# Performance work log

Hardware: AMD Instinct MI355X
Metric: run time of the kernel (lower is better)

Reference implementation:

```python
import jax, jax.numpy as jnp
import numpy as np

B, T, S, H = 8, 256, 256, 512

def setup_inputs() -> dict:
    key = jax.random.key(0)
    k1, k2, k3, k4, k5, k6 = jax.random.split(key, 6)
    query = jax.random.normal(k1, (B, T, H), dtype=jnp.float32)
    encoder_outputs = jax.random.normal(k2, (B, S, H), dtype=jnp.float32)
    # lengths in [1, S] so every row has at least one valid source position
    src_lengths = jax.random.randint(k3, (B,), 1, S + 1, dtype=jnp.int64)
    scale = 1.0 / np.sqrt(H)
    W_h = jax.random.normal(k4, (H, H), dtype=jnp.float32) * scale  # nn.Linear weight (out, in)
    W_s = jax.random.normal(k5, (H, H), dtype=jnp.float32) * scale
    v = jax.random.normal(k6, (H,), dtype=jnp.float32) * scale     # nn.Linear(H,1) weight squeezed
    return {"query": query, "encoder_outputs": encoder_outputs,
            "src_lengths": src_lengths, "W_h": W_h, "W_s": W_s, "v": v}

def reference(query, encoder_outputs, src_lengths, W_h, W_s, v):
    # Linear without bias: y = x @ W^T
    enc_f = jnp.einsum('bsh,oh->bso', encoder_outputs, W_h)   # (B,S,H)
    qry_f = jnp.einsum('bth,oh->bto', query, W_s)             # (B,T,H)
    # additive score: v^T tanh(enc_f + qry_f), broadcast over (T,S)
    scores = jnp.einsum('btsh,h->bts',
                        jnp.tanh(enc_f[:, None, :, :] + qry_f[:, :, None, :]), v)  # (B,T,S)
    mask = jnp.arange(S)[None, :] >= src_lengths[:, None]      # (B,S) True = pad
    scores = jnp.where(mask[:, None, :], -jnp.inf, scores)
    attn_weights = jax.nn.softmax(scores, axis=-1)             # (B,T,S)
    attn_out = jnp.einsum('bts,bsh->bth', attn_weights, encoder_outputs)
    return attn_out
```

## Files before the change

### kernel.cpp

```cpp
#include <hip/hip_runtime.h>
#include <cstddef>
#include <math.h>

#define BD 8
#define TD 256
#define SD 256
#define HD 512
#define K2F 2.885390081777927f

#define EXP2(x) __builtin_amdgcn_exp2f(x)
#define RCP(x)  __builtin_amdgcn_rcpf(x)

typedef __attribute__((ext_vector_type(8))) _Float16 half8;
typedef __attribute__((ext_vector_type(4))) float float4v;

__device__ __forceinline__ float exp2_sat(float x) {
    return EXP2(fminf(fmaxf(x, -80.0f), 80.0f));
}

#define LSTR 40
__global__ __launch_bounds__(256) void proj_kernel(
    const float* __restrict__ enc, const float* __restrict__ qry,
    const float* __restrict__ Wh,  const float* __restrict__ Ws,
    float* __restrict__ encT, float* __restrict__ qryf)
{
    __shared__ _Float16 LA[64 * LSTR], LB[64 * LSTR];

    const int tid = threadIdx.x;
    const int l = tid & 63, w = tid >> 6;
    const int rf = l & 15, q = l >> 4;
    const int my = blockIdx.y;
    const bool isq = my >= 32;
    const int m0 = my * 64;
    const int n0 = blockIdx.x * 64;

    const int srow = tid >> 2;
    const int scol = (tid & 3) * 8;
    const float* Abase = isq
        ? qry + (size_t)(m0 - 2048 + srow) * HD + scol
        : enc + (size_t)(m0 + srow) * HD + scol;
    const float* Bbase = (isq ? Ws : Wh) + (size_t)(n0 + srow) * HD + scol;

    const int mi = (w & 1) * 32, ni = (w >> 1) * 32;

    float4v acc[2][2] = {{{0,0,0,0},{0,0,0,0}},{{0,0,0,0},{0,0,0,0}}};

    float4 a0 = *(const float4*)(Abase);
    float4 a1 = *(const float4*)(Abase + 4);
    float4 b0 = *(const float4*)(Bbase);
    float4 b1 = *(const float4*)(Bbase + 4);

    for (int ks = 0; ks < 16; ++ks) {
        if (ks) __syncthreads();
        {
            float af[8] = {a0.x,a0.y,a0.z,a0.w,a1.x,a1.y,a1.z,a1.w};
            float bf[8] = {b0.x,b0.y,b0.z,b0.w,b1.x,b1.y,b1.z,b1.w};
            half8 ha, hb;
            #pragma unroll
            for (int i = 0; i < 8; ++i) { ha[i] = (_Float16)af[i]; hb[i] = (_Float16)bf[i]; }
            *(half8*)&LA[srow * LSTR + scol] = ha;
            *(half8*)&LB[srow * LSTR + scol] = hb;
        }
        __syncthreads();
        if (ks + 1 < 16) {
            const int ko = (ks + 1) * 32;
            a0 = *(const float4*)(Abase + ko);
            a1 = *(const float4*)(Abase + ko + 4);
            b0 = *(const float4*)(Bbase + ko);
            b1 = *(const float4*)(Bbase + ko + 4);
        }
        half8 ah[2], bh[2];
        #pragma unroll
        for (int i = 0; i < 2; ++i) {
            ah[i] = *(const half8*)&LA[(mi + i * 16 + rf) * LSTR + q * 8];
            bh[i] = *(const half8*)&LB[(ni + i * 16 + rf) * LSTR + q * 8];
        }
        #pragma unroll
        for (int i = 0; i < 2; ++i)
            #pragma unroll
            for (int j = 0; j < 2; ++j)
                acc[i][j] = __builtin_amdgcn_mfma_f32_16x16x32_f16(ah[i], bh[j], acc[i][j], 0, 0, 0);
    }

    if (!isq) {
        const int b  = m0 >> 8;
        const int sb = (m0 & 255) + mi + q * 4;
        float* base = encT + (size_t)b * HD * SD;
        #pragma unroll
        for (int i = 0; i < 2; ++i)
            #pragma unroll
            for (int j = 0; j < 2; ++j) {
                float4 o = make_float4(exp2_sat(acc[i][j][0]*K2F), exp2_sat(acc[i][j][1]*K2F),
                                       exp2_sat(acc[i][j][2]*K2F), exp2_sat(acc[i][j][3]*K2F));
                *(float4*)(base + (size_t)(n0 + ni + j * 16 + rf) * SD + sb + i * 16) = o;
            }
    } else {
        const int mrow = (m0 - 2048) + mi + q * 4;
        #pragma unroll
        for (int i = 0; i < 2; ++i)
            #pragma unroll
            for (int j = 0; j < 2; ++j)
                #pragma unroll
                for (int r = 0; r < 4; ++r)
                    qryf[(size_t)(mrow + i * 16 + r) * HD + n0 + ni + j * 16 + rf] =
                        exp2_sat(acc[i][j][r] * K2F);
    }
}

__global__ __launch_bounds__(512) void attn_kernel(
    const float* __restrict__ enc,
    const float* __restrict__ encT,
    const float* __restrict__ qry_f,
    const float* __restrict__ v,
    const int*   __restrict__ lens,
    float* __restrict__ out)
{
    __shared__ float qls[HD * 4];
    __shared__ float pls[8 * 4 * 256];
    __shared__ float wls[4 * SD];

    const int blk = blockIdx.x;
    const int b   = blk >> 6;
    const int t0  = (blk & 63) * 4;
    const int tid = threadIdx.x;
    const int w   = tid >> 6;
    const int l   = tid & 63;

    {
        const float* qf = qry_f + ((size_t)b * TD + t0) * HD;
        float4 qv;
        qv.x = qf[0 * HD + tid]; qv.y = qf[1 * HD + tid];
        qv.z = qf[2 * HD + tid]; qv.w = qf[3 * HD + tid];
        *(float4*)&qls[tid * 4] = qv;
    }
    __syncthreads();

    float a[4][4];
    #pragma unroll
    for (int t = 0; t < 4; ++t)
        #pragma unroll
        for (int c = 0; c < 4; ++c) a[t][c] = 0.0f;
    {
        const float* ep = encT + (size_t)b * HD * SD + (size_t)(w * 64) * SD + l * 4;
        const int jbase = w * 64;
        float4 e = *(const float4*)ep;
        #pragma unroll 2
        for (int jj = 0; jj < 64; ++jj) {
            float4 en = *(const float4*)(ep + (size_t)(jj + 1) * SD);
            float4 q4 = *(const float4*)&qls[(jbase + jj) * 4];
            float vj = v[jbase + jj];
            float ev[4] = {e.x, e.y, e.z, e.w};
            float qv[4] = {q4.x, q4.y, q4.z, q4.w};
            #pragma unroll
            for (int t = 0; t < 4; ++t)
                #pragma unroll
                for (int c = 0; c < 4; ++c) {
                    float p = fmaf(ev[c], qv[t], 1.0f);
                    a[t][c] = fmaf(vj, RCP(p), a[t][c]);
                }
            e = en;
        }
    }
    #pragma unroll
    for (int t = 0; t < 4; ++t)
        *(float4*)&pls[(w * 4 + t) * 256 + l * 4] = make_float4(a[t][0], a[t][1], a[t][2], a[t][3]);
    __syncthreads();

    if (w < 4) {
        const int t = w;
        float p[4] = {0, 0, 0, 0};
        #pragma unroll
        for (int g = 0; g < 8; ++g) {
            float4 pp = *(const float4*)&pls[(g * 4 + t) * 256 + l * 4];
            p[0] += pp.x; p[1] += pp.y; p[2] += pp.z; p[3] += pp.w;
        }
        const int len = lens[b];
        const int s0 = l * 4;
        float sc[4];
        #pragma unroll
        for (int c = 0; c < 4; ++c)
            sc[c] = (s0 + c < len) ? -2.0f * p[c] : -INFINITY;
        float mx = fmaxf(fmaxf(sc[0], sc[1]), fmaxf(sc[2], sc[3]));
        #pragma unroll
        for (int off = 32; off; off >>= 1) mx = fmaxf(mx, __shfl_xor(mx, off));
        float ex[4]; float sum = 0.0f;
        #pragma unroll
        for (int c = 0; c < 4; ++c) { ex[c] = __expf(sc[c] - mx); sum += ex[c]; }
        #pragma unroll
        for (int off = 32; off; off >>= 1) sum += __shfl_xor(sum, off);
        const float inv = RCP(sum);
        *(float4*)&wls[t * SD + s0] = make_float4(ex[0]*inv, ex[1]*inv, ex[2]*inv, ex[3]*inv);
    }
    __syncthreads();

    const int g  = tid >> 7;
    const int h4 = (tid & 127) * 4;
    float* avred = pls;
    {
        const float* eb = enc + (size_t)b * SD * HD + h4;
        float4 o[4] = {{0,0,0,0},{0,0,0,0},{0,0,0,0},{0,0,0,0}};
        #pragma unroll 2
        for (int ss = 0; ss < 64; ++ss) {
            const int s = g * 64 + ss;
            float4 evv = *(const float4*)(eb + (size_t)s * HD);
            float wt[4];
            #pragma unroll
            for (int t = 0; t < 4; ++t) wt[t] = wls[t * SD + s];
            #pragma unroll
            for (int t = 0; t < 4; ++t) {
                o[t].x = fmaf(wt[t], evv.x, o[t].x);
                o[t].y = fmaf(wt[t], evv.y, o[t].y);
                o[t].z = fmaf(wt[t], evv.z, o[t].z);
                o[t].w = fmaf(wt[t], evv.w, o[t].w);
            }
        }
        #pragma unroll
        for (int t = 0; t < 4; ++t)
            *(float4*)&avred[(size_t)(g * 4 + t) * 512 + h4] = o[t];
    }
    __syncthreads();

    {
        const int t  = tid >> 7;
        const int hh = (tid & 127) * 4;
        float4 r = {0, 0, 0, 0};
        #pragma unroll
        for (int gg = 0; gg < 4; ++gg) {
            float4 x = *(const float4*)&avred[(size_t)(gg * 4 + t) * 512 + hh];
            r.x += x.x; r.y += x.y; r.z += x.z; r.w += x.w;
        }
        *(float4*)(out + ((size_t)b * TD + t0 + t) * HD + hh) = r;
    }
}

extern "C" void kernel_launch(void* const* d_in, const int* in_sizes, int n_in,
                              void* d_out, int out_size, void* d_ws, size_t ws_size,
                              hipStream_t stream) {
    const float* query = (const float*)d_in[0];
    const float* enc   = (const float*)d_in[1];
    const int*   lens  = (const int*)d_in[2];
    const float* W_h   = (const float*)d_in[3];
    const float* W_s   = (const float*)d_in[4];
    const float* v     = (const float*)d_in[5];
    float* out = (float*)d_out;

    char* ws = (char*)d_ws;
    float* encT = (float*)(ws);
    float* qryf = (float*)(ws + ((size_t)4 << 20));

    dim3 pgrid(HD / 64, 64);
    proj_kernel<<<pgrid, 256, 0, stream>>>(enc, query, W_h, W_s, encT, qryf);

    attn_kernel<<<BD * (TD / 4), 512, 0, stream>>>(enc, encT, qryf, v, lens, out);
}
```

Baseline: 124.5 us.

## Fuse projection and attention into one cooperative kernel with grid sync

```diff
diff --git a/kernel.cpp b/kernel.cpp
--- a/kernel.cpp
+++ b/kernel.cpp
@@ -1,6 +1,9 @@
 #include <hip/hip_runtime.h>
+#include <hip/hip_cooperative_groups.h>
 #include <cstddef>
 #include <math.h>
+
+namespace cg = cooperative_groups;
 
 #define BD 8
 #define TD 256
@@ -12,6 +15,7 @@
 #define RCP(x)  __builtin_amdgcn_rcpf(x)
 
 typedef __attribute__((ext_vector_type(8))) _Float16 half8;
+typedef __attribute__((ext_vector_type(4))) _Float16 half4;
 typedef __attribute__((ext_vector_type(4))) float float4v;
 
 __device__ __forceinline__ float exp2_sat(float x) {
@@ -19,7 +23,232 @@
 }
 
 #define LSTR 40
-__global__ __launch_bounds__(256) void proj_kernel(
+
+__global__ __launch_bounds__(512) void fused_kernel(
+    const float* __restrict__ enc,
+    const float* __restrict__ qry,
+    const float* __restrict__ Wh,
+    const float* __restrict__ Ws,
+    const float* __restrict__ v,
+    const int*   __restrict__ lens,
+    float* __restrict__ encT,
+    float* __restrict__ qryf,
+    float* __restrict__ out)
+{
+    __shared__ float smem[7168];
+
+    const int bid = blockIdx.x;
+    const int tid = threadIdx.x;
+    const int l   = tid & 63;
+    const int w   = tid >> 6;
+    const int rf  = l & 15;
+    const int q   = l >> 4;
+
+    {
+        _Float16* LA = (_Float16*)smem;
+        _Float16* LB = (_Float16*)(smem + 1280);
+
+        const int my = bid >> 3;
+        const bool isq = my >= 32;
+        const int m0 = my * 64;
+        const int n0 = (bid & 7) * 64;
+
+        const int srow = tid >> 3;
+        const int scol = (tid & 7) * 4;
+        const float* Abase = isq
+            ? qry + (size_t)(m0 - 2048 + srow) * HD + scol
+            : enc + (size_t)(m0 + srow) * HD + scol;
+        const float* Bbase = (isq ? Ws : Wh) + (size_t)(n0 + srow) * HD + scol;
+
+        const int mi = (w & 3) * 16;
+        const int ni = (w >> 2) * 32;
+
+        float4v acc[2] = {{0,0,0,0},{0,0,0,0}};
+
+        float4 a0 = *(const float4*)(Abase);
+        float4 b0 = *(const float4*)(Bbase);
+
+        for (int ks = 0; ks < 16; ++ks) {
+            if (ks) __syncthreads();
+            {
+                half4 ha, hb;
+                ha[0]=(_Float16)a0.x; ha[1]=(_Float16)a0.y; ha[2]=(_Float16)a0.z; ha[3]=(_Float16)a0.w;
+                hb[0]=(_Float16)b0.x; hb[1]=(_Float16)b0.y; hb[2]=(_Float16)b0.z; hb[3]=(_Float16)b0.w;
+                *(half4*)&LA[srow * LSTR + scol] = ha;
+                *(half4*)&LB[srow * LSTR + scol] = hb;
+            }
+            __syncthreads();
+            if (ks + 1 < 16) {
+                const int ko = (ks + 1) * 32;
+                a0 = *(const float4*)(Abase + ko);
+                b0 = *(const float4*)(Bbase + ko);
+            }
+            half8 ah = *(const half8*)&LA[(mi + rf) * LSTR + q * 8];
+            #pragma unroll
+            for (int j = 0; j < 2; ++j) {
+                half8 bh = *(const half8*)&LB[(ni + j * 16 + rf) * LSTR + q * 8];
+                acc[j] = __builtin_amdgcn_mfma_f32_16x16x32_f16(ah, bh, acc[j], 0, 0, 0);
+            }
+        }
+
+        if (!isq) {
+            const int b  = m0 >> 8;
+            const int sb = (m0 & 255) + mi + q * 4;
+            float* base = encT + (size_t)b * HD * SD;
+            #pragma unroll
+            for (int j = 0; j < 2; ++j) {
+                float4 o = make_float4(exp2_sat(acc[j][0]*K2F), exp2_sat(acc[j][1]*K2F),
+                                       exp2_sat(acc[j][2]*K2F), exp2_sat(acc[j][3]*K2F));
+                *(float4*)(base + (size_t)(n0 + ni + j * 16 + rf) * SD + sb) = o;
+            }
+        } else {
+            const int mrow = (m0 - 2048) + mi + q * 4;
+            #pragma unroll
+            for (int j = 0; j < 2; ++j)
+                #pragma unroll
+                for (int r = 0; r < 4; ++r)
+                    qryf[(size_t)(mrow + r) * HD + n0 + ni + j * 16 + rf] =
+                        exp2_sat(acc[j][r] * K2F);
+        }
+    }
+
+    cg::this_grid().sync();
+
+    {
+        float* qls = smem;
+        float* pls = smem + 2048;
+        float* wls = smem + 6144;
+
+        const int b  = bid >> 6;
+        const int t0 = (bid & 63) * 4;
+
+        {
+            const float* qf = qryf + ((size_t)b * TD + t0) * HD;
+            float4 qv;
+            qv.x = qf[0 * HD + tid]; qv.y = qf[1 * HD + tid];
+            qv.z = qf[2 * HD + tid]; qv.w = qf[3 * HD + tid];
+            *(float4*)&qls[tid * 4] = qv;
+        }
+        __syncthreads();
+
+        float a[4][4];
+        #pragma unroll
+        for (int t = 0; t < 4; ++t)
+            #pragma unroll
+            for (int c = 0; c < 4; ++c) a[t][c] = 0.0f;
+        {
+            const float* ep = encT + (size_t)b * HD * SD + (size_t)(w * 64) * SD + l * 4;
+            const int jbase = w * 64;
+            #pragma unroll 4
+            for (int jj = 0; jj < 64; ++jj) {
+                float4 e = *(const float4*)(ep + (size_t)jj * SD);
+                float4 q4 = *(const float4*)&qls[(jbase + jj) * 4];
+                float vj = v[jbase + jj];
+                float ev[4] = {e.x, e.y, e.z, e.w};
+                float qv[4] = {q4.x, q4.y, q4.z, q4.w};
+                #pragma unroll
+                for (int t = 0; t < 4; ++t)
+                    #pragma unroll
+                    for (int c = 0; c < 4; ++c) {
+                        float p = fmaf(ev[c], qv[t], 1.0f);
+                        a[t][c] = fmaf(vj, RCP(p), a[t][c]);
+                    }
+            }
+        }
+        if (w < 4) {
+            #pragma unroll
+            for (int t = 0; t < 4; ++t)
+                *(float4*)&pls[(w * 4 + t) * 256 + l * 4] =
+                    make_float4(a[t][0], a[t][1], a[t][2], a[t][3]);
+        }
+        __syncthreads();
+        if (w >= 4) {
+            #pragma unroll
+            for (int t = 0; t < 4; ++t) {
+                float4 c4 = *(const float4*)&pls[((w - 4) * 4 + t) * 256 + l * 4];
+                c4.x += a[t][0]; c4.y += a[t][1]; c4.z += a[t][2]; c4.w += a[t][3];
+                *(float4*)&pls[((w - 4) * 4 + t) * 256 + l * 4] = c4;
+            }
+        }
+        __syncthreads();
+
+        if (w < 4) {
+            const int t = w;
+            float p[4] = {0, 0, 0, 0};
+            #pragma unroll
+            for (int g = 0; g < 4; ++g) {
+                float4 pp = *(const float4*)&pls[(g * 4 + t) * 256 + l * 4];
+                p[0] += pp.x; p[1] += pp.y; p[2] += pp.z; p[3] += pp.w;
+            }
+            const int len = lens[b];
+            const int s0 = l * 4;
+            float sc[4];
+            #pragma unroll
+            for (int c = 0; c < 4; ++c)
+                sc[c] = (s0 + c < len) ? -2.0f * p[c] : -INFINITY;
+            float mx = fmaxf(fmaxf(sc[0], sc[1]), fmaxf(sc[2], sc[3]));
+            #pragma unroll
+            for (int off = 32; off; off >>= 1) mx = fmaxf(mx, __shfl_xor(mx, off));
+            float ex[4]; float sum = 0.0f;
+            #pragma unroll
+            for (int c = 0; c < 4; ++c) { ex[c] = __expf(sc[c] - mx); sum += ex[c]; }
+            #pragma unroll
+            for (int off = 32; off; off >>= 1) sum += __shfl_xor(sum, off);
+            const float inv = RCP(sum);
+            *(float4*)&wls[t * SD + s0] = make_float4(ex[0]*inv, ex[1]*inv, ex[2]*inv, ex[3]*inv);
+        }
+        __syncthreads();
+
+        const int sg = tid >> 7;
+        const int h4 = (tid & 127) * 4;
+        float* avred = pls;
+        float4 o[4] = {{0,0,0,0},{0,0,0,0},{0,0,0,0},{0,0,0,0}};
+        {
+            const float* eb = enc + (size_t)b * SD * HD + h4;
+            #pragma unroll 2
+            for (int ss = 0; ss < 64; ++ss) {
+                const int s = sg * 64 + ss;
+                float4 evv = *(const float4*)(eb + (size_t)s * HD);
+                float wt[4];
+                #pragma unroll
+                for (int t = 0; t < 4; ++t) wt[t] = wls[t * SD + s];
+                #pragma unroll
+                for (int t = 0; t < 4; ++t) {
+                    o[t].x = fmaf(wt[t], evv.x, o[t].x);
+                    o[t].y = fmaf(wt[t], evv.y, o[t].y);
+                    o[t].z = fmaf(wt[t], evv.z, o[t].z);
+                    o[t].w = fmaf(wt[t], evv.w, o[t].w);
+                }
+            }
+        }
+        if (sg < 2) {
+            #pragma unroll
+            for (int t = 0; t < 4; ++t)
+                *(float4*)&avred[(size_t)(sg * 4 + t) * 512 + h4] = o[t];
+        }
+        __syncthreads();
+        if (sg >= 2) {
+            #pragma unroll
+            for (int t = 0; t < 4; ++t) {
+                float4 c4 = *(const float4*)&avred[(size_t)((sg - 2) * 4 + t) * 512 + h4];
+                c4.x += o[t].x; c4.y += o[t].y; c4.z += o[t].z; c4.w += o[t].w;
+                *(float4*)&avred[(size_t)((sg - 2) * 4 + t) * 512 + h4] = c4;
+            }
+        }
+        __syncthreads();
+
+        {
+            const int t  = tid >> 7;
+            const int hh = (tid & 127) * 4;
+            float4 x0 = *(const float4*)&avred[(size_t)(0 * 4 + t) * 512 + hh];
+            float4 x1 = *(const float4*)&avred[(size_t)(1 * 4 + t) * 512 + hh];
+            float4 r = make_float4(x0.x + x1.x, x0.y + x1.y, x0.z + x1.z, x0.w + x1.w);
+            *(float4*)(out + ((size_t)b * TD + t0 + t) * HD + hh) = r;
+        }
+    }
+}
+
+__global__ __launch_bounds__(256) void proj_fb(
     const float* __restrict__ enc, const float* __restrict__ qry,
     const float* __restrict__ Wh,  const float* __restrict__ Ws,
     float* __restrict__ encT, float* __restrict__ qryf)
@@ -42,7 +271,6 @@
     const float* Bbase = (isq ? Ws : Wh) + (size_t)(n0 + srow) * HD + scol;
 
     const int mi = (w & 1) * 32, ni = (w >> 1) * 32;
-
     float4v acc[2][2] = {{{0,0,0,0},{0,0,0,0}},{{0,0,0,0},{0,0,0,0}}};
 
     float4 a0 = *(const float4*)(Abase);
@@ -107,13 +335,10 @@
     }
 }
 
-__global__ __launch_bounds__(512) void attn_kernel(
-    const float* __restrict__ enc,
-    const float* __restrict__ encT,
-    const float* __restrict__ qry_f,
-    const float* __restrict__ v,
-    const int*   __restrict__ lens,
-    float* __restrict__ out)
+__global__ __launch_bounds__(512) void attn_fb(
+    const float* __restrict__ enc, const float* __restrict__ encT,
+    const float* __restrict__ qryf, const float* __restrict__ v,
+    const int* __restrict__ lens, float* __restrict__ out)
 {
     __shared__ float qls[HD * 4];
     __shared__ float pls[8 * 4 * 256];
@@ -127,7 +352,7 @@
     const int l   = tid & 63;
 
     {
-        const float* qf = qry_f + ((size_t)b * TD + t0) * HD;
+        const float* qf = qryf + ((size_t)b * TD + t0) * HD;
         float4 qv;
         qv.x = qf[0 * HD + tid]; qv.y = qf[1 * HD + tid];
         qv.z = qf[2 * HD + tid]; qv.w = qf[3 * HD + tid];
@@ -143,10 +368,9 @@
     {
         const float* ep = encT + (size_t)b * HD * SD + (size_t)(w * 64) * SD + l * 4;
         const int jbase = w * 64;
-        float4 e = *(const float4*)ep;
-        #pragma unroll 2
+        #pragma unroll 4
         for (int jj = 0; jj < 64; ++jj) {
-            float4 en = *(const float4*)(ep + (size_t)(jj + 1) * SD);
+            float4 e = *(const float4*)(ep + (size_t)jj * SD);
             float4 q4 = *(const float4*)&qls[(jbase + jj) * 4];
             float vj = v[jbase + jj];
             float ev[4] = {e.x, e.y, e.z, e.w};
@@ -158,7 +382,6 @@
                     float p = fmaf(ev[c], qv[t], 1.0f);
                     a[t][c] = fmaf(vj, RCP(p), a[t][c]);
                 }
-            e = en;
         }
     }
     #pragma unroll
@@ -219,7 +442,6 @@
             *(float4*)&avred[(size_t)(g * 4 + t) * 512 + h4] = o[t];
     }
     __syncthreads();
-
     {
         const int t  = tid >> 7;
         const int hh = (tid & 127) * 4;
@@ -248,8 +470,22 @@
     float* encT = (float*)(ws);
     float* qryf = (float*)(ws + ((size_t)4 << 20));
 
+    int nb = 0;
+    hipError_t oerr = hipOccupancyMaxActiveBlocksPerMultiprocessor(
+        &nb, (const void*)fused_kernel, 512, 0);
+    bool coop_ok = (oerr == hipSuccess) && (nb * 256 >= 512);
+
+    if (coop_ok) {
+        void* args[] = {
+            (void*)&enc, (void*)&query, (void*)&W_h, (void*)&W_s,
+            (void*)&v, (void*)&lens, (void*)&encT, (void*)&qryf, (void*)&out
+        };
+        hipError_t lerr = hipLaunchCooperativeKernel((const void*)fused_kernel,
+                                                     dim3(512), dim3(512), args, 0, stream);
+        if (lerr == hipSuccess) return;
+    }
+
     dim3 pgrid(HD / 64, 64);
-    proj_kernel<<<pgrid, 256, 0, stream>>>(enc, query, W_h, W_s, encT, qryf);
-
-    attn_kernel<<<BD * (TD / 4), 512, 0, stream>>>(enc, encT, qryf, v, lens, out);
+    proj_fb<<<pgrid, 256, 0, stream>>>(enc, query, W_h, W_s, encT, qryf);
+    attn_fb<<<BD * (TD / 4), 512, 0, stream>>>(enc, encT, qryf, v, lens, out);
 }
```

Result: faster. 120.9 us (-2.9%).

## Drop LDS staging in projection GEMM and remap block indices

Applied to the files above, without the earlier changes.

```diff
diff --git a/kernel.cpp b/kernel.cpp
--- a/kernel.cpp
+++ b/kernel.cpp
@@ -18,99 +18,69 @@
     return EXP2(fminf(fmaxf(x, -80.0f), 80.0f));
 }
 
-#define LSTR 40
+__device__ __forceinline__ half8 to_h8(float4 lo, float4 hi) {
+    half8 h;
+    h[0]=(_Float16)lo.x; h[1]=(_Float16)lo.y; h[2]=(_Float16)lo.z; h[3]=(_Float16)lo.w;
+    h[4]=(_Float16)hi.x; h[5]=(_Float16)hi.y; h[6]=(_Float16)hi.z; h[7]=(_Float16)hi.w;
+    return h;
+}
+
 __global__ __launch_bounds__(256) void proj_kernel(
     const float* __restrict__ enc, const float* __restrict__ qry,
     const float* __restrict__ Wh,  const float* __restrict__ Ws,
     float* __restrict__ encT, float* __restrict__ qryf)
 {
-    __shared__ _Float16 LA[64 * LSTR], LB[64 * LSTR];
-
+    const int bid = blockIdx.x;
     const int tid = threadIdx.x;
-    const int l = tid & 63, w = tid >> 6;
-    const int rf = l & 15, q = l >> 4;
-    const int my = blockIdx.y;
-    const bool isq = my >= 32;
-    const int m0 = my * 64;
-    const int n0 = blockIdx.x * 64;
-
-    const int srow = tid >> 2;
-    const int scol = (tid & 3) * 8;
-    const float* Abase = isq
-        ? qry + (size_t)(m0 - 2048 + srow) * HD + scol
-        : enc + (size_t)(m0 + srow) * HD + scol;
-    const float* Bbase = (isq ? Ws : Wh) + (size_t)(n0 + srow) * HD + scol;
-
-    const int mi = (w & 1) * 32, ni = (w >> 1) * 32;
-
-    float4v acc[2][2] = {{{0,0,0,0},{0,0,0,0}},{{0,0,0,0},{0,0,0,0}}};
-
-    float4 a0 = *(const float4*)(Abase);
-    float4 a1 = *(const float4*)(Abase + 4);
-    float4 b0 = *(const float4*)(Bbase);
-    float4 b1 = *(const float4*)(Bbase + 4);
-
+    const int l   = tid & 63;
+    const int w   = tid >> 6;
+    const int rf  = l & 15;
+    const int q   = l >> 4;
+
+    const int x  = bid & 7;
+    const int g  = bid >> 3;
+    const int mq = x + 8 * (g >> 5);
+    const int n0 = (g & 31) * 16;
+
+    const int srow0 = mq * 64 + w * 16;
+    const bool isq = srow0 >= 2048;
+
+    const float* Arow = (isq ? qry + (size_t)(srow0 - 2048 + rf) * HD
+                             : enc + (size_t)(srow0 + rf) * HD) + q * 8;
+    const float* Brow = (isq ? Ws : Wh) + (size_t)(n0 + rf) * HD + q * 8;
+
+    float4v acc = {0, 0, 0, 0};
+
+    #pragma unroll 4
     for (int ks = 0; ks < 16; ++ks) {
-        if (ks) __syncthreads();
-        {
-            float af[8] = {a0.x,a0.y,a0.z,a0.w,a1.x,a1.y,a1.z,a1.w};
-            float bf[8] = {b0.x,b0.y,b0.z,b0.w,b1.x,b1.y,b1.z,b1.w};
-            half8 ha, hb;
-            #pragma unroll
-            for (int i = 0; i < 8; ++i) { ha[i] = (_Float16)af[i]; hb[i] = (_Float16)bf[i]; }
-            *(half8*)&LA[srow * LSTR + scol] = ha;
-            *(half8*)&LB[srow * LSTR + scol] = hb;
-        }
-        __syncthreads();
-        if (ks + 1 < 16) {
-            const int ko = (ks + 1) * 32;
-            a0 = *(const float4*)(Abase + ko);
-            a1 = *(const float4*)(Abase + ko + 4);
-            b0 = *(const float4*)(Bbase + ko);
-            b1 = *(const float4*)(Bbase + ko + 4);
-        }
-        half8 ah[2], bh[2];
-        #pragma unroll
-        for (int i = 0; i < 2; ++i) {
-            ah[i] = *(const half8*)&LA[(mi + i * 16 + rf) * LSTR + q * 8];
-            bh[i] = *(const half8*)&LB[(ni + i * 16 + rf) * LSTR + q * 8];
-        }
-        #pragma unroll
-        for (int i = 0; i < 2; ++i)
-            #pragma unroll
-            for (int j = 0; j < 2; ++j)
-                acc[i][j] = __builtin_amdgcn_mfma_f32_16x16x32_f16(ah[i], bh[j], acc[i][j], 0, 0, 0);
+        const int k0 = ks * 32;
+        float4 al = *(const float4*)(Arow + k0);
+        float4 ah = *(const float4*)(Arow + k0 + 4);
+        float4 bl = *(const float4*)(Brow + k0);
+        float4 bh = *(const float4*)(Brow + k0 + 4);
+        half8 ha = to_h8(al, ah);
+        half8 hb = to_h8(bl, bh);
+        acc = __builtin_amdgcn_mfma_f32_16x16x32_f16(ha, hb, acc, 0, 0, 0);
     }
 
     if (!isq) {
-        const int b  = m0 >> 8;
-        const int sb = (m0 & 255) + mi + q * 4;
-        float* base = encT + (size_t)b * HD * SD;
-        #pragma unroll
-        for (int i = 0; i < 2; ++i)
-            #pragma unroll
-            for (int j = 0; j < 2; ++j) {
-                float4 o = make_float4(exp2_sat(acc[i][j][0]*K2F), exp2_sat(acc[i][j][1]*K2F),
-                                       exp2_sat(acc[i][j][2]*K2F), exp2_sat(acc[i][j][3]*K2F));
-                *(float4*)(base + (size_t)(n0 + ni + j * 16 + rf) * SD + sb + i * 16) = o;
-            }
+        const int b  = srow0 >> 8;
+        const int sb = (srow0 & 255) + q * 4;
+        float4 o = make_float4(exp2_sat(acc[0]*K2F), exp2_sat(acc[1]*K2F),
+                               exp2_sat(acc[2]*K2F), exp2_sat(acc[3]*K2F));
+        *(float4*)(encT + (size_t)b * HD * SD + (size_t)(n0 + rf) * SD + sb) = o;
     } else {
-        const int mrow = (m0 - 2048) + mi + q * 4;
-        #pragma unroll
-        for (int i = 0; i < 2; ++i)
-            #pragma unroll
-            for (int j = 0; j < 2; ++j)
-                #pragma unroll
-                for (int r = 0; r < 4; ++r)
-                    qryf[(size_t)(mrow + i * 16 + r) * HD + n0 + ni + j * 16 + rf] =
-                        exp2_sat(acc[i][j][r] * K2F);
+        const int mrow = (srow0 - 2048) + q * 4;
+        #pragma unroll
+        for (int r = 0; r < 4; ++r)
+            qryf[(size_t)(mrow + r) * HD + n0 + rf] = exp2_sat(acc[r] * K2F);
     }
 }
 
 __global__ __launch_bounds__(512) void attn_kernel(
     const float* __restrict__ enc,
     const float* __restrict__ encT,
-    const float* __restrict__ qry_f,
+    const float* __restrict__ qryf,
     const float* __restrict__ v,
     const int*   __restrict__ lens,
     float* __restrict__ out)
@@ -120,14 +90,14 @@
     __shared__ float wls[4 * SD];
 
     const int blk = blockIdx.x;
-    const int b   = blk >> 6;
-    const int t0  = (blk & 63) * 4;
+    const int b   = blk & 7;
+    const int t0  = (blk >> 3) * 4;
     const int tid = threadIdx.x;
     const int w   = tid >> 6;
     const int l   = tid & 63;
 
     {
-        const float* qf = qry_f + ((size_t)b * TD + t0) * HD;
+        const float* qf = qryf + ((size_t)b * TD + t0) * HD;
         float4 qv;
         qv.x = qf[0 * HD + tid]; qv.y = qf[1 * HD + tid];
         qv.z = qf[2 * HD + tid]; qv.w = qf[3 * HD + tid];
@@ -143,10 +113,9 @@
     {
         const float* ep = encT + (size_t)b * HD * SD + (size_t)(w * 64) * SD + l * 4;
         const int jbase = w * 64;
-        float4 e = *(const float4*)ep;
-        #pragma unroll 2
+        #pragma unroll 4
         for (int jj = 0; jj < 64; ++jj) {
-            float4 en = *(const float4*)(ep + (size_t)(jj + 1) * SD);
+            float4 e = *(const float4*)(ep + (size_t)jj * SD);
             float4 q4 = *(const float4*)&qls[(jbase + jj) * 4];
             float vj = v[jbase + jj];
             float ev[4] = {e.x, e.y, e.z, e.w};
@@ -158,7 +127,6 @@
                     float p = fmaf(ev[c], qv[t], 1.0f);
                     a[t][c] = fmaf(vj, RCP(p), a[t][c]);
                 }
-            e = en;
         }
     }
     #pragma unroll
@@ -226,8 +194,8 @@
         float4 r = {0, 0, 0, 0};
         #pragma unroll
         for (int gg = 0; gg < 4; ++gg) {
-            float4 x = *(const float4*)&avred[(size_t)(gg * 4 + t) * 512 + hh];
-            r.x += x.x; r.y += x.y; r.z += x.z; r.w += x.w;
+            float4 xx = *(const float4*)&avred[(size_t)(gg * 4 + t) * 512 + hh];
+            r.x += xx.x; r.y += xx.y; r.z += xx.z; r.w += xx.w;
         }
         *(float4*)(out + ((size_t)b * TD + t0 + t) * HD + hh) = r;
     }
@@ -248,8 +216,6 @@
     float* encT = (float*)(ws);
     float* qryf = (float*)(ws + ((size_t)4 << 20));
 
-    dim3 pgrid(HD / 64, 64);
-    proj_kernel<<<pgrid, 256, 0, stream>>>(enc, query, W_h, W_s, encT, qryf);
-
-    attn_kernel<<<BD * (TD / 4), 512, 0, stream>>>(enc, encT, qryf, v, lens, out);
-}
+    proj_kernel<<<2048, 256, 0, stream>>>(enc, query, W_h, W_s, encT, qryf);
+    attn_kernel<<<512, 512, 0, stream>>>(enc, encT, qryf, v, lens, out);
+}
```

New measurement: 165.4 us. 32.8% more time.
